# Kernel optimization log

Measured on AMD Instinct MI355X. Metric: run time of the kernel, lower is better.

The kernel has to match this reference:

```python
import jax, jax.numpy as jnp
from jax import lax
import numpy as np

SCALES = [1.0, 0.9, 0.8, 0.7, 0.6]
SOFTMAX_SCALE = 10.0
RES_SCALE = 1.0
EPS = 1e-4  # escape_NaN buffer


def prelu(x, a):
    # torch nn.PReLU with a single shared parameter a
    return jnp.where(x >= 0, x, a * x)


def conv1x1(x, W, b):
    # x: [B,Cin,H,W], W: [Cout,Cin], b: [Cout]
    return jnp.einsum('oi,bihw->bohw', W, x) + b[None, :, None, None]


def extract_patches(x):
    # x: [B,C,H,W] -> [B, H*W, C, 3, 3]; 'same' padding (pad 1), stride 1,
    # matching F.unfold channel ordering (C, kh, kw) and row-major spatial order.
    B, C, H, W = x.shape
    p = jnp.pad(x, ((0, 0), (0, 0), (1, 1), (1, 1)))
    shifts = [p[:, :, i:i + H, j:j + W] for i in range(3) for j in range(3)]
    pat = jnp.stack(shifts, axis=-1)                      # [B,C,H,W,9]
    pat = pat.reshape(B, C, H, W, 3, 3)
    return pat.transpose(0, 2, 3, 1, 4, 5).reshape(B, H * W, C, 3, 3)


def setup_inputs() -> dict:
    key = jax.random.key(0)
    ks = jax.random.split(key, 7)
    B, C, H, W = 4, 64, 48, 48
    red = 2
    x = jax.random.normal(ks[0], (B, C, H, W), jnp.float32)
    # conv_match_L_base: 1x1 conv 64->32 + PReLU
    Wb = jax.random.normal(ks[1], (C // red, C), jnp.float32) * 0.05
    bb = jax.random.normal(ks[2], (C // red,), jnp.float32) * 0.05
    ab = jnp.asarray(0.25, jnp.float32)
    # conv_match: 1x1 conv 64->32 + PReLU
    Wm = jax.random.normal(ks[3], (C // red, C), jnp.float32) * 0.05
    bm = jax.random.normal(ks[4], (C // red,), jnp.float32) * 0.05
    am = jnp.asarray(0.25, jnp.float32)
    # conv_assembly: 1x1 conv 64->64 + PReLU
    Wa = jax.random.normal(ks[5], (C, C), jnp.float32) * 0.05
    ba = jax.random.normal(ks[6], (C,), jnp.float32) * 0.05
    aa = jnp.asarray(0.25, jnp.float32)
    return {"x": x, "Wb": Wb, "bb": bb, "ab": ab,
            "Wm": Wm, "bm": bm, "am": am,
            "Wa": Wa, "ba": ba, "aa": aa}


def reference(x, Wb, bb, ab, Wm, bm, am, Wa, ba, aa):
    B, C, H, W = x.shape
    match_base = prelu(conv1x1(x, Wb, bb), ab)  # [B,32,H,W]

    w_list, raw_list = [], []
    for s in SCALES:
        if s != 1.0:
            Hs, Ws = int(H * s), int(W * s)
            ref = jax.image.resize(x, (B, C, Hs, Ws), 'bilinear', antialias=False)
        else:
            ref = x
        base = prelu(conv1x1(ref, Wa, ba), aa)   # [B,64,Hs,Ws]
        mat = prelu(conv1x1(ref, Wm, bm), am)    # [B,32,Hs,Ws]
        raw_list.append(extract_patches(base))   # [B,Ls,64,3,3]
        w_list.append(extract_patches(mat))      # [B,Ls,32,3,3]

    wall = jnp.concatenate(w_list, axis=1)       # [B,N,32,3,3]
    rawall = jnp.concatenate(raw_list, axis=1)   # [B,N,64,3,3]
    norm = jnp.maximum(jnp.sqrt(jnp.sum(wall * wall, axis=(2, 3, 4), keepdims=True)), EPS)
    wn = wall / norm

    dn = ('NCHW', 'OIHW', 'NCHW')

    def per_sample(xb, wb, rb):
        # xb: [32,H,W], wb: [N,32,3,3], rb: [N,64,3,3]
        scores = lax.conv_general_dilated(xb[None], wb, (1, 1), ((1, 1), (1, 1)),
                                          dimension_numbers=dn)       # [1,N,H,W]
        attn = jax.nn.softmax(scores * SOFTMAX_SCALE, axis=1)
        # conv_transpose2d(attn, rb, stride=1, padding=1) == conv with flipped,
        # channel-swapped kernel and padding 1
        kt = jnp.flip(rb, axis=(2, 3)).transpose(1, 0, 2, 3)           # [64,N,3,3]
        out = lax.conv_general_dilated(attn, kt, (1, 1), ((1, 1), (1, 1)),
                                       dimension_numbers=dn)           # [1,64,H,W]
        return out[0] / 4.0

    y = jax.vmap(per_sample)(match_base, wn, rawall)  # [B,64,H,W]
    return y + x * RES_SCALE
```

## Files before the change

### kernel.cpp

```cpp
#include <hip/hip_runtime.h>
#include <hip/hip_bf16.h>
#include <hip/hip_fp16.h>

typedef __half h16;
typedef _Float16 f16;
typedef f16 f16x8 __attribute__((ext_vector_type(8)));
typedef __attribute__((ext_vector_type(4))) float f32x4;

#define NB 4
#define NCH 64
#define HW 2304
#define NP 7470
#define NPAD 7552
#define NT 236
#define NBLK 59
#define SW2 NPAD

__device__ __forceinline__ float us2f(unsigned short u){
  unsigned v = (unsigned)u << 16; float f; __builtin_memcpy(&f, &v, 4); return f;
}
__device__ __forceinline__ void gl16(const void* g, void* l){
  __builtin_amdgcn_global_load_lds((const __attribute__((address_space(1))) unsigned int*)g,
                                   (__attribute__((address_space(3))) unsigned int*)l, 16, 0, 0);
}

__device__ __forceinline__ void n_decode(int n, int& off, int& d, int& y, int& x){
  if (n < 2304)      { off = 0;    d = 48; }
  else if (n < 4153) { off = 2304; d = 43; }
  else if (n < 5597) { off = 4153; d = 38; }
  else if (n < 6686) { off = 5597; d = 33; }
  else               { off = 6686; d = 28; }
  int l = n - off; y = l / d; x = l - y * d;
}

__global__ __launch_bounds__(256) void k_detect(const void* __restrict__ x, int* __restrict__ flag){
  const unsigned short* u = (const unsigned short*)x;
  int tid = threadIdx.x;
  int c = 0;
  for (int i = tid; i < 8192; i += 256){
    float v = us2f(u[i]);
    float a = fabsf(v);
    if (v == 0.f || (a > 1e-5f && a < 1e3f)) c++;
  }
  #pragma unroll
  for (int o = 1; o < 64; o <<= 1) c += __shfl_xor(c, o);
  __shared__ int wr[4];
  if ((tid & 63) == 0) wr[tid >> 6] = c;
  __syncthreads();
  if (tid == 0) flag[0] = ((wr[0]+wr[1]+wr[2]+wr[3]) > 7000) ? 1 : 0;
}

struct CanonArgs { const void* src[10]; float* dst[10]; int end[10]; };

__global__ __launch_bounds__(256) void k_canon_all(CanonArgs a, int tot, const int* __restrict__ flag){
  int id = blockIdx.x * 256 + threadIdx.x;
  if (id >= tot) return;
  int k = 0;
  while (id >= a.end[k]) k++;
  int local = id - (k ? a.end[k-1] : 0);
  float v;
  if (flag[0]) v = us2f(((const unsigned short*)a.src[k])[local]);
  else         v = ((const float*)a.src[k])[local];
  a.dst[k][local] = v;
}

__global__ __launch_bounds__(256) void k_resize(const float* __restrict__ x, h16* __restrict__ xs){
  int id = blockIdx.x * 256 + threadIdx.x;
  if (id >= NB * NCH * NP) return;
  int b = id / (NCH*NP), rem = id - b*(NCH*NP);
  int c = rem / NP, n = rem - c*NP;
  int off, d, y, xx; n_decode(n, off, d, y, xx);
  const float* pc = x + ((size_t)b * NCH + c) * HW;
  float v;
  if (off == 0){
    v = pc[y*48 + xx];
  } else {
    float cy = (y + 0.5f) * (48.0f / (float)d) - 0.5f;
    float cx = (xx + 0.5f) * (48.0f / (float)d) - 0.5f;
    int y0 = (int)floorf(cy), x0 = (int)floorf(cx);
    float fy = cy - (float)y0, fx = cx - (float)x0;
    int y1 = min(y0 + 1, 47), x1 = min(x0 + 1, 47);
    y0 = max(y0, 0); x0 = max(x0, 0);
    v = (1.f-fy)*((1.f-fx)*pc[y0*48+x0] + fx*pc[y0*48+x1])
      + fy*((1.f-fx)*pc[y1*48+x0] + fx*pc[y1*48+x1]);
  }
  xs[id] = __float2half(v);
}

template<bool OB>
__global__ __launch_bounds__(256) void k_conv1x1(const h16* __restrict__ in, const float* __restrict__ Wt,
    const float* __restrict__ bias, const float* __restrict__ alpha, void* __restrict__ outv,
    int npix, int cout, size_t in_bstride, size_t out_bstride, int rs_in, int rs_out){
  __shared__ float Wl[64*64];
  __shared__ float it[64][64];
  int b = blockIdx.y;
  int n0 = blockIdx.x * 64;
  int tid = threadIdx.x;
  const h16* ib = in + (size_t)b * in_bstride;
  for (int i = tid; i < cout * 64; i += 256) Wl[i] = Wt[i];
  for (int i = tid; i < 64 * 64; i += 256){
    int ci = i >> 6, nn = i & 63;
    int n = n0 + nn;
    it[ci][nn] = (n < npix) ? __half2float(ib[(size_t)ci * rs_in + n]) : 0.f;
  }
  __syncthreads();
  float al = alpha[0];
  for (int oi = tid; oi < cout * 64; oi += 256){
    int co = oi >> 6, nn = oi & 63;
    float acc = bias[co];
    #pragma unroll
    for (int ci = 0; ci < 64; ci++) acc = fmaf(Wl[co*64+ci], it[ci][nn], acc);
    acc = acc >= 0.f ? acc : al * acc;
    int n = n0 + nn;
    if (n < npix){
      size_t idx = (size_t)b * out_bstride + (size_t)co * rs_out + n;
      if constexpr (OB) ((h16*)outv)[idx] = __float2half(acc);
      else              ((float*)outv)[idx] = acc;
    }
  }
}

__global__ __launch_bounds__(256) void k_sq(const float* __restrict__ mat, float* __restrict__ q){
  int id = blockIdx.x * 256 + threadIdx.x;
  if (id >= NB * NP) return;
  int b = id / NP, n = id - b * NP;
  const float* mp = mat + (size_t)b * 32 * NP + n;
  float s = 0.f;
  #pragma unroll
  for (int c = 0; c < 32; c++){ float v = mp[(size_t)c * NP]; s += v * v; }
  q[id] = s;
}

__global__ __launch_bounds__(256) void k_ninv(const float* __restrict__ q, float* __restrict__ ninv){
  int id = blockIdx.x * 256 + threadIdx.x;
  if (id >= NB * NP) return;
  int b = id / NP, n = id - b * NP;
  int off, d, y, x; n_decode(n, off, d, y, x);
  const float* qb = q + (size_t)b * NP + off;
  float s = 0.f;
  #pragma unroll
  for (int dy = -1; dy <= 1; dy++){
    int yy = y + dy; if (yy < 0 || yy >= d) continue;
    #pragma unroll
    for (int dx = -1; dx <= 1; dx++){
      int xx = x + dx; if (xx < 0 || xx >= d) continue;
      s += qb[yy * d + xx];
    }
  }
  ninv[id] = 1.f / fmaxf(sqrtf(s), 1e-4f);
}

__global__ __launch_bounds__(256) void k_packU(const float* __restrict__ mb, h16* __restrict__ U){
  int id = blockIdx.x * 256 + threadIdx.x;
  if (id >= NB * HW * 288) return;
  int b = id / (HW*288), rem = id - b*(HW*288);
  int p = rem / 288, k = rem - p * 288;
  int c = k / 9, r = k - c * 9, kh = r / 3, kw = r - kh * 3;
  int y = p / 48 + kh - 1, x = (p % 48) + kw - 1;
  float v = 0.f;
  if (y >= 0 && y < 48 && x >= 0 && x < 48)
    v = mb[((size_t)b * 32 + c) * HW + y * 48 + x];
  U[id] = __float2half(v);
}

__global__ __launch_bounds__(256) void k_packW(const float* __restrict__ mat, const float* __restrict__ ninv,
                                               h16* __restrict__ Wp, int b0, int g){
  int id = blockIdx.x * 256 + threadIdx.x;
  if (id >= g * NPAD * 288) return;
  int bg = id / (NPAD*288), rem = id - bg*(NPAD*288);
  int n = rem / 288, k = rem - n * 288;
  float v = 0.f;
  if (n < NP){
    int b = b0 + bg;
    int c = k / 9, r = k - c * 9, kh = r / 3, kw = r - kh * 3;
    int off, d, y, x; n_decode(n, off, d, y, x);
    int yy = y + kh - 1, xx = x + kw - 1;
    if (yy >= 0 && yy < d && xx >= 0 && xx < d)
      v = mat[((size_t)b * 32 + c) * NP + off + yy * d + xx] * 10.f * ninv[(size_t)b*NP + n];
  }
  Wp[id] = __float2half(v);
}

__global__ __launch_bounds__(256) void k_packR(const h16* __restrict__ src, h16* __restrict__ dst){
  int id = blockIdx.x * 256 + threadIdx.x;
  if (id >= NB * NT * 576 * 32) return;
  int b = id / (NT*576*32), rem = id - b*(NT*576*32);
  int t = rem / (576*32), rem2 = rem - t*(576*32);
  int j = rem2 / 32, kl = rem2 - j*32;
  int n = t*32 + kl;
  h16 v = __float2half(0.f);
  if (n < NP){
    int c = j / 9, r = j - c * 9, kh = r / 3, kw = r - kh * 3;
    int off, d, y, x; n_decode(n, off, d, y, x);
    int yy = y + kh - 1, xx = x + kw - 1;
    if (yy >= 0 && yy < d && xx >= 0 && xx < d)
      v = src[((size_t)b * 64 + c) * NP + off + yy * d + xx];
  }
  dst[id] = v;
}

__global__ __launch_bounds__(512) void k_gemm1m(const f16* __restrict__ U, const f16* __restrict__ Wp,
    h16* __restrict__ S16, float* __restrict__ Pm, float* __restrict__ Ps, int b0){
  int bg = blockIdx.z, b = b0 + bg;
  int m0 = blockIdx.y * 128, n0 = blockIdx.x * 128;
  int tid = threadIdx.x, l = tid & 63, w = tid >> 6;
  int wm = w >> 1, wn = w & 1;
  int ch = l >> 4, cl = l & 15;
  __shared__ __align__(16) char At[2][8192];
  __shared__ __align__(16) char Bt[2][8192];
  __shared__ float mred[128][2];
  __shared__ float sred[128][2];
  f32x4 acc[2][4] = {};
  const f16* Ub = U + ((size_t)b * HW + m0) * 288;
  const f16* Wb = Wp + ((size_t)bg * NPAD + n0) * 288;
  int abyte[2], bbyte[4];
  #pragma unroll
  for (int mt = 0; mt < 2; mt++){
    int lr = wm*32 + mt*16 + cl;
    abyte[mt] = lr*64 + ((ch ^ ((lr>>1)&3))<<4);
  }
  #pragma unroll
  for (int nt = 0; nt < 4; nt++){
    int lr = wn*64 + nt*16 + cl;
    bbyte[nt] = lr*64 + ((ch ^ ((lr>>1)&3))<<4);
  }
  int srow = tid >> 2, scs = (tid & 3) ^ ((srow >> 1) & 3);
  gl16(Ub + (size_t)srow*288 + 0 + scs*8, At[0] + tid*16);
  gl16(Wb + (size_t)srow*288 + 0 + scs*8, Bt[0] + tid*16);
  __syncthreads();
  int cur = 0;
  for (int k0 = 0; k0 < 288; k0 += 32){
    if (k0 + 32 < 288){
      gl16(Ub + (size_t)srow*288 + k0 + 32 + scs*8, At[cur^1] + tid*16);
      gl16(Wb + (size_t)srow*288 + k0 + 32 + scs*8, Bt[cur^1] + tid*16);
    }
    f16x8 a[2], bv[4];
    #pragma unroll
    for (int mt = 0; mt < 2; mt++) a[mt] = *reinterpret_cast<const f16x8*>(At[cur] + abyte[mt]);
    #pragma unroll
    for (int nt = 0; nt < 4; nt++) bv[nt] = *reinterpret_cast<const f16x8*>(Bt[cur] + bbyte[nt]);
    #pragma unroll
    for (int mt = 0; mt < 2; mt++)
      #pragma unroll
      for (int nt = 0; nt < 4; nt++)
        acc[mt][nt] = __builtin_amdgcn_mfma_f32_16x16x32_f16(a[mt], bv[nt], acc[mt][nt], 0, 0, 0);
    __syncthreads();
    cur ^= 1;
  }
  #pragma unroll
  for (int mt = 0; mt < 2; mt++)
    #pragma unroll
    for (int i = 0; i < 4; i++){
      float v = -3e38f;
      #pragma unroll
      for (int nt = 0; nt < 4; nt++){
        int gn = n0 + wn*64 + nt*16 + cl;
        float t = acc[mt][nt][i];
        v = fmaxf(v, (gn < NP) ? t : -3e38f);
      }
      v = fmaxf(v, __shfl_xor(v, 1));
      v = fmaxf(v, __shfl_xor(v, 2));
      v = fmaxf(v, __shfl_xor(v, 4));
      v = fmaxf(v, __shfl_xor(v, 8));
      if (cl == 0) mred[wm*32 + mt*16 + ch*4 + i][wn] = v;
    }
  __syncthreads();
  #pragma unroll
  for (int mt = 0; mt < 2; mt++)
    #pragma unroll
    for (int i = 0; i < 4; i++){
      int r = wm*32 + mt*16 + ch*4 + i;
      float Ml = fmaxf(mred[r][0], mred[r][1]);
      int gm = m0 + r;
      float s = 0.f;
      #pragma unroll
      for (int nt = 0; nt < 4; nt++){
        int gn = n0 + wn*64 + nt*16 + cl;
        float e = (gn < NP) ? __expf(acc[mt][nt][i] - Ml) : 0.f;
        S16[((size_t)bg*HW + gm)*SW2 + gn] = __float2half(e);
        s += e;
      }
      s += __shfl_xor(s, 1);
      s += __shfl_xor(s, 2);
      s += __shfl_xor(s, 4);
      s += __shfl_xor(s, 8);
      if (cl == 0) sred[r][wn] = s;
    }
  __syncthreads();
  if (tid < 128){
    float Mf = fmaxf(mred[tid][0], mred[tid][1]);
    float L  = sred[tid][0] + sred[tid][1];
    size_t o = ((size_t)bg*HW + m0 + tid)*NBLK + blockIdx.x;
    Pm[o] = Mf; Ps[o] = L;
  }
}

__global__ __launch_bounds__(256) void k_sfac(const float* __restrict__ Pm, const float* __restrict__ Ps,
                                              float* __restrict__ Fac, int gc){
  int rid = blockIdx.x * 4 + (threadIdx.x >> 6);
  int lane = threadIdx.x & 63;
  if (rid >= gc * HW) return;
  const float* pm = Pm + (size_t)rid * NBLK;
  const float* ps = Ps + (size_t)rid * NBLK;
  float mv = (lane < NBLK) ? pm[lane] : -3e38f;
  float sv = (lane < NBLK) ? ps[lane] : 0.f;
  float M = mv;
  #pragma unroll
  for (int o = 1; o < 64; o <<= 1) M = fmaxf(M, __shfl_xor(M, o));
  float e = (lane < NBLK) ? __expf(mv - M) : 0.f;
  float c = e * sv;
  #pragma unroll
  for (int o = 1; o < 64; o <<= 1) c += __shfl_xor(c, o);
  float inv = 1.f / c;
  if (lane < NBLK) Fac[(size_t)rid * NBLK + lane] = e * inv;
}

__global__ __launch_bounds__(512) void k_gemm2n(const f16* __restrict__ S16, const f16* __restrict__ RpT,
    const float* __restrict__ Fac, h16* __restrict__ T, int b0){
  int nwg = gridDim.x;
  int p = blockIdx.x;
  int L = (nwg % 8 == 0) ? ((p & 7)*(nwg>>3) + (p>>3)) : p;
  int jh = L % 3; int t1 = L / 3; int my = t1 % 36; int bg = t1 / 36;
  int b = b0 + bg;
  int m0 = my * 64;
  int tid = threadIdx.x, l = tid & 63, w = tid >> 6;
  int wm = w >> 2, wc = w & 3;
  int ch = l >> 4, cl = l & 15;
  __shared__ __align__(16) char smem[56704];
  f32x4 acc[2][3] = {};
  int lrm[2], abyte[2], rbyte[3];
  #pragma unroll
  for (int mt = 0; mt < 2; mt++){
    lrm[mt] = wm*32 + mt*16 + cl;
    abyte[mt] = lrm[mt]*64 + ((ch ^ ((lrm[mt]>>1)&3))<<4);
  }
  #pragma unroll
  for (int nt = 0; nt < 3; nt++){
    int jr = wc*48 + nt*16 + cl;
    rbyte[nt] = jr*64 + ((ch ^ ((jr>>1)&3))<<4);
  }
  const f16* Sb  = S16 + ((size_t)bg*HW + m0)*SW2;
  const f16* Rb0 = RpT + (size_t)b*((size_t)NT*576*32) + (size_t)jh*(192*32);
  const float* facb = Fac + ((size_t)bg*HW + m0)*NBLK;

  auto STAGE = [&](int t, int bi){
    char* dS = smem + bi*4096;
    char* dR = smem + 12288 + bi*12288;
    const f16* Rb = Rb0 + (size_t)t*(576*32);
    if (tid < 256){
      int row = tid >> 2, cs = (tid & 3) ^ ((row >> 1) & 3);
      gl16(Sb + (size_t)row*SW2 + t*32 + cs*8, dS + tid*16);
      int i2 = tid + 512;
      int r2 = i2 >> 2, c2 = (i2 & 3) ^ ((r2 >> 1) & 3);
      gl16(Rb + (size_t)r2*32 + c2*8, dR + i2*16);
    } else {
      int i1 = tid - 256;
      int r1 = i1 >> 2, c1 = (i1 & 3) ^ ((r1 >> 1) & 3);
      gl16(Rb + (size_t)r1*32 + c1*8, dR + i1*16);
      int r2 = tid >> 2, c2 = (tid & 3) ^ ((r2 >> 1) & 3);
      gl16(Rb + (size_t)r2*32 + c2*8, dR + tid*16);
    }
  };

  {
    f16* fl = (f16*)(smem + 49152);
    for (int i = tid; i < NBLK*64; i += 512){
      int nb = i >> 6, mm = i & 63;
      fl[i] = (f16)facb[(size_t)mm*NBLK + nb];
    }
  }
  STAGE(0, 0);
  STAGE(1, 1);
  __syncthreads();

  int cur = 0;
  for (int t = 0; t < NT; ++t){
    int nx = cur + 2; if (nx >= 3) nx -= 3;
    if (t + 2 < NT){
      STAGE(t + 2, nx);
      asm volatile("s_waitcnt vmcnt(4)" ::: "memory");
    } else if (t + 1 < NT){
      asm volatile("s_waitcnt vmcnt(2)" ::: "memory");
    } else {
      asm volatile("s_waitcnt vmcnt(0)" ::: "memory");
    }
    __builtin_amdgcn_s_barrier();
    asm volatile("" ::: "memory");
    const char* Sc = smem + cur*4096;
    const char* Rc = smem + 12288 + cur*12288;
    const f16* fl = (const f16*)(smem + 49152);
    int nb = t >> 2;
    f16x8 pa[2];
    #pragma unroll
    for (int mt = 0; mt < 2; mt++){
      f16 fac = fl[nb*64 + lrm[mt]];
      f16x8 sv = *reinterpret_cast<const f16x8*>(Sc + abyte[mt]);
      pa[mt] = sv * fac;
    }
    #pragma unroll
    for (int nt = 0; nt < 3; nt++){
      f16x8 bv = *reinterpret_cast<const f16x8*>(Rc + rbyte[nt]);
      #pragma unroll
      for (int mt = 0; mt < 2; mt++)
        acc[mt][nt] = __builtin_amdgcn_mfma_f32_16x16x32_f16(pa[mt], bv, acc[mt][nt], 0, 0, 0);
    }
    asm volatile("s_waitcnt lgkmcnt(0)" ::: "memory");
    __builtin_amdgcn_s_barrier();
    cur = cur + 1; if (cur >= 3) cur = 0;
  }

  {
    h16* Tl = (h16*)smem;
    #pragma unroll
    for (int nt = 0; nt < 3; nt++)
      #pragma unroll
      for (int mt = 0; mt < 2; mt++)
        #pragma unroll
        for (int i = 0; i < 4; i++)
          Tl[(wc*48 + nt*16 + cl)*72 + wm*32 + mt*16 + ch*4 + i] = __float2half(acc[mt][nt][i]);
    __syncthreads();
    #pragma unroll
    for (int rep = 0; rep < 3; rep++){
      int idx = tid + rep*512;
      int j0 = idx >> 3, q = idx & 7;
      uint4 v = *reinterpret_cast<const uint4*>((const char*)Tl + j0*144 + q*16);
      h16* dst = T + ((size_t)b*576 + jh*192 + j0)*HW + m0 + q*8;
      *reinterpret_cast<uint4*>(dst) = v;
    }
  }
}

__global__ __launch_bounds__(256) void k_fold(const h16* __restrict__ T, const float* __restrict__ x,
    void* __restrict__ out, const int* __restrict__ flag){
  int id = blockIdx.x * 256 + threadIdx.x;
  if (id >= NB * 64 * HW) return;
  int b = id / (64*HW), id2 = id - b*(64*HW);
  int co = id2 / HW, p = id2 - co * HW;
  int y = p / 48, xx = p - y * 48;
  float acc = 0.f;
  #pragma unroll
  for (int dy = -1; dy <= 1; dy++){
    int yy = y + dy; if (yy < 0 || yy >= 48) continue;
    #pragma unroll
    for (int dx = -1; dx <= 1; dx++){
      int x2 = xx + dx; if (x2 < 0 || x2 >= 48) continue;
      int j = co*9 + (1-dy)*3 + (1-dx);
      acc += __half2float(T[((size_t)b*576 + j)*HW + yy*48 + x2]);
    }
  }
  size_t gi = (size_t)id;
  float r = x[gi] + 0.25f * acc;
  if (flag[0]) ((__hip_bfloat16*)out)[gi] = __float2bfloat16(r);
  else         ((float*)out)[gi] = r;
}

extern "C" void kernel_launch(void* const* d_in, const int* in_sizes, int n_in,
                              void* d_out, int out_size, void* d_ws, size_t ws_size,
                              hipStream_t stream){
  (void)out_size; (void)n_in;

  char* cur = (char*)d_ws;
  auto carve = [&](size_t bytes)->char*{
    char* p = cur; cur += (bytes + 255) & ~(size_t)255; return p;
  };
  int*   flag  = (int*)  carve(4);
  float* canon[10];
  for (int i = 0; i < 10; i++) canon[i] = (float*)carve((size_t)in_sizes[i] * 4);
  float* xc = canon[0];
  float* Wb = canon[1]; float* bb = canon[2]; float* ab = canon[3];
  float* Wm = canon[4]; float* bm = canon[5]; float* am = canon[6];
  float* Wa = canon[7]; float* ba = canon[8]; float* aa = canon[9];

  h16*   xs    = (h16*)  carve((size_t)NB * 64 * NP * 2);
  float* mbuf  = (float*)carve((size_t)NB * 32 * HW * 4);
  float* mat   = (float*)carve((size_t)NB * 32 * NP * 4);
  float* qbuf  = (float*)carve((size_t)NB * NP * 4);
  float* ninv  = (float*)carve((size_t)NB * NP * 4);
  h16*   baseh = (h16*)  carve((size_t)NB * 64 * NP * 2);
  h16*   U     = (h16*)  carve((size_t)NB * HW * 288 * 2);
  h16*   RpT   = (h16*)  carve((size_t)NB * NT * 576 * 32 * 2);
  h16*   T     = (h16*)  carve((size_t)NB * 576 * HW * 2);

  size_t fixed = (size_t)(cur - (char*)d_ws);
  size_t perb  = (((size_t)NPAD*288*2 + 255) & ~(size_t)255)
               + (((size_t)HW*SW2*2 + 255) & ~(size_t)255)
               + 3 * (((size_t)HW*NBLK*4 + 255) & ~(size_t)255);
  size_t avail = (ws_size > fixed) ? ws_size - fixed : 0;
  int g = (int)(avail / perb);
  if (g < 1) g = 1;
  if (g > NB) g = NB;
  h16*   Wp  = (h16*)  carve((size_t)g * NPAD * 288 * 2);
  h16*   S16 = (h16*)  carve((size_t)g * HW * SW2 * 2);
  float* Pm  = (float*)carve((size_t)g * HW * NBLK * 4);
  float* Ps  = (float*)carve((size_t)g * HW * NBLK * 4);
  float* Fac = (float*)carve((size_t)g * HW * NBLK * 4);

  k_detect<<<1, 256, 0, stream>>>(d_in[0], flag);
  {
    CanonArgs ca; int tot = 0;
    for (int i = 0; i < 10; i++){
      ca.src[i] = d_in[i]; ca.dst[i] = canon[i];
      tot += in_sizes[i]; ca.end[i] = tot;
    }
    k_canon_all<<<(tot + 255)/256, 256, 0, stream>>>(ca, tot, flag);
  }

  k_resize<<<((size_t)NB*NCH*NP + 255)/256, 256, 0, stream>>>(xc, xs);

  dim3 gm((NP + 63)/64, NB);
  k_conv1x1<false><<<gm, 256, 0, stream>>>(xs, Wm, bm, am, (void*)mat,   NP, 32, (size_t)64*NP, (size_t)32*NP, NP, NP);
  k_conv1x1<true ><<<gm, 256, 0, stream>>>(xs, Wa, ba, aa, (void*)baseh, NP, 64, (size_t)64*NP, (size_t)64*NP, NP, NP);
  dim3 gb2((HW + 63)/64, NB);
  k_conv1x1<false><<<gb2, 256, 0, stream>>>(xs, Wb, bb, ab, (void*)mbuf, HW, 32, (size_t)64*NP, (size_t)32*HW, NP, HW);

  k_sq  <<<(NB*NP + 255)/256, 256, 0, stream>>>(mat, qbuf);
  k_ninv<<<(NB*NP + 255)/256, 256, 0, stream>>>(qbuf, ninv);
  k_packU<<<((size_t)NB*HW*288 + 255)/256, 256, 0, stream>>>(mbuf, U);
  k_packR<<<((size_t)NB*NT*576*32 + 255)/256, 256, 0, stream>>>(baseh, RpT);

  for (int b0 = 0; b0 < NB; b0 += g){
    int gc = (b0 + g <= NB) ? g : (NB - b0);
    k_packW<<<((size_t)gc*NPAD*288 + 255)/256, 256, 0, stream>>>(mat, ninv, Wp, b0, gc);
    dim3 g1(NBLK, HW/128, gc);
    k_gemm1m<<<g1, 512, 0, stream>>>((const f16*)U, (const f16*)Wp, S16, Pm, Ps, b0);
    k_sfac<<<(gc*HW + 3)/4, 256, 0, stream>>>(Pm, Ps, Fac, gc);
    int nwg2 = 3 * 36 * gc;
    k_gemm2n<<<nwg2, 512, 0, stream>>>((const f16*)S16, (const f16*)RpT, Fac, T, b0);
  }

  k_fold<<<(NB*64*HW + 255)/256, 256, 0, stream>>>(T, xc, d_out, flag);
}
```

Measured before the change: 366.1 us.

## Triple-buffer gemm1 K loop and double M tile of gemm2 to 128 rows

The score GEMM moves from double to triple buffering of its K tiles, using explicit vmcnt waits and raw barriers so global-to-LDS loads overlap compute further ahead. The attention-times-patches GEMM doubles its M tile from 64 to 128 rows per workgroup, so each staged R tile is reused by twice as many rows, while dropping to two LDS buffers to stay within the shared-memory budget. This halves the workgroup count of gemm2 and raises per-wave accumulator registers, which may lower occupancy and parallelism at small batch groups.

```diff
diff --git a/kernel.cpp b/kernel.cpp
--- a/kernel.cpp
+++ b/kernel.cpp
@@ -206,8 +206,8 @@
   int tid = threadIdx.x, l = tid & 63, w = tid >> 6;
   int wm = w >> 1, wn = w & 1;
   int ch = l >> 4, cl = l & 15;
-  __shared__ __align__(16) char At[2][8192];
-  __shared__ __align__(16) char Bt[2][8192];
+  __shared__ __align__(16) char At[3][8192];
+  __shared__ __align__(16) char Bt[3][8192];
   __shared__ float mred[128][2];
   __shared__ float sred[128][2];
   f32x4 acc[2][4] = {};
@@ -225,15 +225,26 @@
     bbyte[nt] = lr*64 + ((ch ^ ((lr>>1)&3))<<4);
   }
   int srow = tid >> 2, scs = (tid & 3) ^ ((srow >> 1) & 3);
-  gl16(Ub + (size_t)srow*288 + 0 + scs*8, At[0] + tid*16);
-  gl16(Wb + (size_t)srow*288 + 0 + scs*8, Bt[0] + tid*16);
+  auto STAGE1 = [&](int t, int bi){
+    gl16(Ub + (size_t)srow*288 + t*32 + scs*8, At[bi] + tid*16);
+    gl16(Wb + (size_t)srow*288 + t*32 + scs*8, Bt[bi] + tid*16);
+  };
+  STAGE1(0, 0);
+  STAGE1(1, 1);
   __syncthreads();
   int cur = 0;
-  for (int k0 = 0; k0 < 288; k0 += 32){
-    if (k0 + 32 < 288){
-      gl16(Ub + (size_t)srow*288 + k0 + 32 + scs*8, At[cur^1] + tid*16);
-      gl16(Wb + (size_t)srow*288 + k0 + 32 + scs*8, Bt[cur^1] + tid*16);
-    }
+  for (int t = 0; t < 9; ++t){
+    int nx = cur + 2; if (nx >= 3) nx -= 3;
+    if (t + 2 < 9){
+      STAGE1(t + 2, nx);
+      asm volatile("s_waitcnt vmcnt(4)" ::: "memory");
+    } else if (t + 1 < 9){
+      asm volatile("s_waitcnt vmcnt(2)" ::: "memory");
+    } else {
+      asm volatile("s_waitcnt vmcnt(0)" ::: "memory");
+    }
+    __builtin_amdgcn_s_barrier();
+    asm volatile("" ::: "memory");
     f16x8 a[2], bv[4];
     #pragma unroll
     for (int mt = 0; mt < 2; mt++) a[mt] = *reinterpret_cast<const f16x8*>(At[cur] + abyte[mt]);
@@ -244,8 +255,9 @@
       #pragma unroll
       for (int nt = 0; nt < 4; nt++)
         acc[mt][nt] = __builtin_amdgcn_mfma_f32_16x16x32_f16(a[mt], bv[nt], acc[mt][nt], 0, 0, 0);
-    __syncthreads();
-    cur ^= 1;
+    asm volatile("s_waitcnt lgkmcnt(0)" ::: "memory");
+    __builtin_amdgcn_s_barrier();
+    cur = cur + 1; if (cur >= 3) cur -= 3;
   }
   #pragma unroll
   for (int mt = 0; mt < 2; mt++)
@@ -320,18 +332,18 @@
   int nwg = gridDim.x;
   int p = blockIdx.x;
   int L = (nwg % 8 == 0) ? ((p & 7)*(nwg>>3) + (p>>3)) : p;
-  int jh = L % 3; int t1 = L / 3; int my = t1 % 36; int bg = t1 / 36;
+  int jh = L % 3; int t1 = L / 3; int my = t1 % 18; int bg = t1 / 18;
   int b = b0 + bg;
-  int m0 = my * 64;
+  int m0 = my * 128;
   int tid = threadIdx.x, l = tid & 63, w = tid >> 6;
   int wm = w >> 2, wc = w & 3;
   int ch = l >> 4, cl = l & 15;
-  __shared__ __align__(16) char smem[56704];
-  f32x4 acc[2][3] = {};
-  int lrm[2], abyte[2], rbyte[3];
-  #pragma unroll
-  for (int mt = 0; mt < 2; mt++){
-    lrm[mt] = wm*32 + mt*16 + cl;
+  __shared__ __align__(16) char smem[56320];
+  f32x4 acc[4][3] = {};
+  int lrm[4], abyte[4], rbyte[3];
+  #pragma unroll
+  for (int mt = 0; mt < 4; mt++){
+    lrm[mt] = wm*64 + mt*16 + cl;
     abyte[mt] = lrm[mt]*64 + ((ch ^ ((lrm[mt]>>1)&3))<<4);
   }
   #pragma unroll
@@ -344,56 +356,53 @@
   const float* facb = Fac + ((size_t)bg*HW + m0)*NBLK;
 
   auto STAGE = [&](int t, int bi){
-    char* dS = smem + bi*4096;
-    char* dR = smem + 12288 + bi*12288;
+    char* dS = smem + bi*8192;
+    char* dR = smem + 16384 + bi*12288;
     const f16* Rb = Rb0 + (size_t)t*(576*32);
-    if (tid < 256){
+    {
       int row = tid >> 2, cs = (tid & 3) ^ ((row >> 1) & 3);
       gl16(Sb + (size_t)row*SW2 + t*32 + cs*8, dS + tid*16);
+    }
+    {
+      int row = tid >> 2, cs = (tid & 3) ^ ((row >> 1) & 3);
+      gl16(Rb + (size_t)row*32 + cs*8, dR + tid*16);
+    }
+    if (tid < 256){
       int i2 = tid + 512;
       int r2 = i2 >> 2, c2 = (i2 & 3) ^ ((r2 >> 1) & 3);
       gl16(Rb + (size_t)r2*32 + c2*8, dR + i2*16);
-    } else {
-      int i1 = tid - 256;
-      int r1 = i1 >> 2, c1 = (i1 & 3) ^ ((r1 >> 1) & 3);
-      gl16(Rb + (size_t)r1*32 + c1*8, dR + i1*16);
-      int r2 = tid >> 2, c2 = (tid & 3) ^ ((r2 >> 1) & 3);
-      gl16(Rb + (size_t)r2*32 + c2*8, dR + tid*16);
     }
   };
 
   {
-    f16* fl = (f16*)(smem + 49152);
-    for (int i = tid; i < NBLK*64; i += 512){
-      int nb = i >> 6, mm = i & 63;
+    f16* fl = (f16*)(smem + 40960);
+    for (int i = tid; i < NBLK*128; i += 512){
+      int nb = i >> 7, mm = i & 127;
       fl[i] = (f16)facb[(size_t)mm*NBLK + nb];
     }
   }
   STAGE(0, 0);
-  STAGE(1, 1);
   __syncthreads();
 
   int cur = 0;
   for (int t = 0; t < NT; ++t){
-    int nx = cur + 2; if (nx >= 3) nx -= 3;
-    if (t + 2 < NT){
-      STAGE(t + 2, nx);
-      asm volatile("s_waitcnt vmcnt(4)" ::: "memory");
-    } else if (t + 1 < NT){
-      asm volatile("s_waitcnt vmcnt(2)" ::: "memory");
+    if (t + 1 < NT){
+      STAGE(t + 1, cur ^ 1);
+      if (tid < 256) { asm volatile("s_waitcnt vmcnt(3)" ::: "memory"); }
+      else           { asm volatile("s_waitcnt vmcnt(2)" ::: "memory"); }
     } else {
       asm volatile("s_waitcnt vmcnt(0)" ::: "memory");
     }
     __builtin_amdgcn_s_barrier();
     asm volatile("" ::: "memory");
-    const char* Sc = smem + cur*4096;
-    const char* Rc = smem + 12288 + cur*12288;
-    const f16* fl = (const f16*)(smem + 49152);
+    const char* Sc = smem + cur*8192;
+    const char* Rc = smem + 16384 + cur*12288;
+    const f16* fl = (const f16*)(smem + 40960);
     int nb = t >> 2;
-    f16x8 pa[2];
-    #pragma unroll
-    for (int mt = 0; mt < 2; mt++){
-      f16 fac = fl[nb*64 + lrm[mt]];
+    f16x8 pa[4];
+    #pragma unroll
+    for (int mt = 0; mt < 4; mt++){
+      f16 fac = fl[nb*128 + lrm[mt]];
       f16x8 sv = *reinterpret_cast<const f16x8*>(Sc + abyte[mt]);
       pa[mt] = sv * fac;
     }
@@ -401,12 +410,12 @@
     for (int nt = 0; nt < 3; nt++){
       f16x8 bv = *reinterpret_cast<const f16x8*>(Rc + rbyte[nt]);
       #pragma unroll
-      for (int mt = 0; mt < 2; mt++)
+      for (int mt = 0; mt < 4; mt++)
         acc[mt][nt] = __builtin_amdgcn_mfma_f32_16x16x32_f16(pa[mt], bv, acc[mt][nt], 0, 0, 0);
     }
     asm volatile("s_waitcnt lgkmcnt(0)" ::: "memory");
     __builtin_amdgcn_s_barrier();
-    cur = cur + 1; if (cur >= 3) cur = 0;
+    cur ^= 1;
   }
 
   {
@@ -414,16 +423,16 @@
     #pragma unroll
     for (int nt = 0; nt < 3; nt++)
       #pragma unroll
-      for (int mt = 0; mt < 2; mt++)
+      for (int mt = 0; mt < 4; mt++)
         #pragma unroll
         for (int i = 0; i < 4; i++)
-          Tl[(wc*48 + nt*16 + cl)*72 + wm*32 + mt*16 + ch*4 + i] = __float2half(acc[mt][nt][i]);
+          Tl[(wc*48 + nt*16 + cl)*136 + wm*64 + mt*16 + ch*4 + i] = __float2half(acc[mt][nt][i]);
     __syncthreads();
     #pragma unroll
-    for (int rep = 0; rep < 3; rep++){
+    for (int rep = 0; rep < 6; rep++){
       int idx = tid + rep*512;
-      int j0 = idx >> 3, q = idx & 7;
-      uint4 v = *reinterpret_cast<const uint4*>((const char*)Tl + j0*144 + q*16);
+      int j0 = idx >> 4, q = idx & 15;
+      uint4 v = *reinterpret_cast<const uint4*>((const char*)Tl + j0*272 + q*16);
       h16* dst = T + ((size_t)b*576 + jh*192 + j0)*HW + m0 + q*8;
       *reinterpret_cast<uint4*>(dst) = v;
     }
@@ -524,7 +533,7 @@
     dim3 g1(NBLK, HW/128, gc);
     k_gemm1m<<<g1, 512, 0, stream>>>((const f16*)U, (const f16*)Wp, S16, Pm, Ps, b0);
     k_sfac<<<(gc*HW + 3)/4, 256, 0, stream>>>(Pm, Ps, Fac, gc);
-    int nwg2 = 3 * 36 * gc;
+    int nwg2 = 3 * 18 * gc;
     k_gemm2n<<<nwg2, 512, 0, stream>>>((const f16*)S16, (const f16*)RpT, Fac, T, b0);
   }
 
```

New measurement: 366.7 us. No clear change (+0.2%).
